# Kernel optimization log

Hardware: AMD Instinct MI355X
Metric: run time of the kernel (lower is better)

## Reference

```python
import jax, jax.numpy as jnp
import numpy as np

B, L, C, H = 8, 2048, 256, 4
D = C // H  # head_dim = 64
EPS = 1e-5


def setup_inputs() -> dict:
    key = jax.random.key(0)
    ks = jax.random.split(key, 16)
    s = lambda fan_in: 1.0 / np.sqrt(fan_in)
    inp = {
        'x0': jax.random.normal(ks[0], (B, L, C), jnp.float32),
        'x1': jax.random.normal(ks[1], (B, L, C), jnp.float32),
        # attention projections (stored as (in, out); torch Linear is x @ W.T + b)
        'Wqk': jax.random.normal(ks[2], (C, C), jnp.float32) * s(C),
        'bqk': jax.random.normal(ks[3], (C,), jnp.float32) * s(C),
        'Wv': jax.random.normal(ks[4], (C, C), jnp.float32) * s(C),
        'bv': jax.random.normal(ks[5], (C,), jnp.float32) * s(C),
        'Wout': jax.random.normal(ks[6], (C, C), jnp.float32) * s(C),
        'bout': jax.random.normal(ks[7], (C,), jnp.float32) * s(C),
        # shared FFN: Linear(2C->2C) -> LayerNorm -> GELU -> Linear(2C->C)
        'W1': jax.random.normal(ks[8], (2 * C, 2 * C), jnp.float32) * s(2 * C),
        'b1': jax.random.normal(ks[9], (2 * C,), jnp.float32) * s(2 * C),
        'ln_g': jnp.ones((2 * C,), jnp.float32),
        'ln_b': jnp.zeros((2 * C,), jnp.float32),
        'W2': jax.random.normal(ks[10], (2 * C, C), jnp.float32) * s(2 * C),
        'b2': jax.random.normal(ks[11], (C,), jnp.float32) * s(2 * C),
    }
    return inp


def _heads(t):
    # (B, L, C) -> (B, H, L, D)
    b, l, _ = t.shape
    return t.reshape(b, l, H, D).transpose(0, 2, 1, 3)


def _merge(t):
    # (B, H, L, D) -> (B, L, C)
    b, h, l, d = t.shape
    return t.transpose(0, 2, 1, 3).reshape(b, l, h * d)


def _ffn(z, W1, b1, ln_g, ln_b, W2, b2):
    h = z @ W1 + b1
    mu = jnp.mean(h, axis=-1, keepdims=True)
    var = jnp.var(h, axis=-1, keepdims=True)
    h = (h - mu) * jax.lax.rsqrt(var + EPS) * ln_g + ln_b
    h = jax.nn.gelu(h, approximate=False)
    return h @ W2 + b2


def reference(x0, x1, Wqk, bqk, Wv, bv, Wout, bout, W1, b1, ln_g, ln_b, W2, b2):
    scale_sqrt = D ** (-0.25)  # sqrt(head_dim**-0.5), applied to both sides
    qk0 = _heads(x0 @ Wqk + bqk) * scale_sqrt  # (B,H,M,D)
    qk1 = _heads(x1 @ Wqk + bqk) * scale_sqrt  # (B,H,N,D)
    v0 = _heads(x0 @ Wv + bv)
    v1 = _heads(x1 @ Wv + bv)

    # single shared similarity matrix (LightGlue trick)
    sim = jnp.einsum('bhid,bhjd->bhij', qk0, qk1)  # (B,H,M,N)
    attn01 = jax.nn.softmax(sim, axis=-1)           # rows: A->B
    attn10 = jax.nn.softmax(sim, axis=-2)           # cols: B->A (softmax of sim^T along last dim)
    m0 = jnp.einsum('bhij,bhjd->bhid', attn01, v1)  # (B,H,M,D)
    m1 = jnp.einsum('bhij,bhid->bhjd', attn10, v0)  # (B,H,N,D)

    m0 = _merge(m0) @ Wout + bout
    m1 = _merge(m1) @ Wout + bout

    x0_out = x0 + _ffn(jnp.concatenate([x0, m0], axis=-1), W1, b1, ln_g, ln_b, W2, b2)
    x1_out = x1 + _ffn(jnp.concatenate([x1, m1], axis=-1), W1, b1, ln_g, ln_b, W2, b2)
    return (x0_out, x1_out)
```

## Files before the change

### kernel.cpp

```cpp
#include <hip/hip_runtime.h>
#include <hip/hip_bf16.h>

typedef _Float16 f16;
typedef _Float16 f16x8 __attribute__((ext_vector_type(8)));
typedef _Float16 f16x4 __attribute__((ext_vector_type(4)));
typedef float f32x4 __attribute__((ext_vector_type(4)));

#define MFMA16(a, b, c) __builtin_amdgcn_mfma_f32_16x16x32_f16((a), (b), (c), 0, 0, 0)
#define MFMA16K16(a, b, c) __builtin_amdgcn_mfma_f32_16x16x16f16((a), (b), (c), 0, 0, 0)

__device__ __forceinline__ void load16(const void* g, void* l) {
    __builtin_amdgcn_global_load_lds((const __attribute__((address_space(1))) void*)g,
                                     (__attribute__((address_space(3))) void*)l, 16, 0, 0);
}

__global__ __launch_bounds__(256) void k_prep(const float* __restrict__ x0,
                                              const float* __restrict__ x1,
                                              const float* __restrict__ Wqk,
                                              const float* __restrict__ Wv,
                                              const float* __restrict__ W1,
                                              const float* __restrict__ W2,
                                              const float* __restrict__ Wout,
                                              const float* __restrict__ b1,
                                              const float* __restrict__ bout,
                                              f16* __restrict__ xh, f16* __restrict__ wcat_t,
                                              f16* __restrict__ w1t, f16* __restrict__ w1bt,
                                              f16* __restrict__ w2t, f16* __restrict__ woutf16,
                                              float* __restrict__ bias_eff) {
    __shared__ float red[4];
    const int blk = blockIdx.x, tid = threadIdx.x;
    if (blk < 8192) {
        size_t i = ((size_t)blk * 256 + tid) * 4;
        const float* src = (i < 4194304) ? (x0 + i) : (x1 + (i - 4194304));
        float4 v = *(const float4*)src;
        f16x4 o = {(f16)v.x, (f16)v.y, (f16)v.z, (f16)v.w};
        *(f16x4*)(xh + i) = o;
    } else if (blk < 8704) {
        int n = blk - 8192;
        const float* W = (n < 256) ? Wqk : Wv;
        wcat_t[n * 256 + tid] = (f16)W[tid * 256 + (n & 255)];
    } else if (blk < 9216) {
        int n = blk - 8704;
        w1t[n * 512 + tid] = (f16)W1[tid * 512 + n];
    } else if (blk < 9728) {
        int n = blk - 9216;
        w1bt[n * 256 + tid] = (f16)W1[(256 + tid) * 512 + n];
    } else if (blk < 10240) {
        int j = blk - 9728;
        int n = j >> 1, k = (j & 1) * 256 + tid;
        w2t[n * 512 + k] = (f16)W2[k * 256 + n];
    } else if (blk < 10496) {
        int o = (blk - 10240) * 256 + tid;
        woutf16[o] = (f16)Wout[o];
    } else {
        int n = blk - 10496;
        float s = bout[tid] * W1[(size_t)(256 + tid) * 512 + n];
#pragma unroll
        for (int off = 1; off < 64; off <<= 1) s += __shfl_xor(s, off);
        int wave = tid >> 6, lane = tid & 63;
        if (lane == 0) red[wave] = s;
        __syncthreads();
        if (tid == 0) bias_eff[n] = b1[n] + red[0] + red[1] + red[2] + red[3];
    }
}

__global__ __launch_bounds__(256) void k_gemm(const f16* __restrict__ A1,
                                              const f16* __restrict__ A2, int ksplit,
                                              int strideA, const f16* __restrict__ Bt, int K,
                                              int N, const float* __restrict__ bias1,
                                              const float* __restrict__ bias2, int mode,
                                              void* __restrict__ out1, void* __restrict__ out2,
                                              const float* __restrict__ res1,
                                              const float* __restrict__ res2) {
    const int bn0 = blockIdx.x * 128;
    const int bm0 = blockIdx.y * 128;
    __shared__ f16 As[2][4096];
    __shared__ f16 Bs[2][4096];
    const int tid = threadIdx.x;
    const int lane = tid & 63, wave = tid >> 6;
    const int quad = lane >> 4, l16 = lane & 15;
    const int wm0 = (wave & 1) * 64, wn0 = (wave >> 1) * 64;
    const int axor = l16 & 3;

    f32x4 acc[4][4];
#pragma unroll
    for (int tm = 0; tm < 4; tm++)
#pragma unroll
        for (int tn = 0; tn < 4; tn++) acc[tm][tn] = (f32x4){0.f, 0.f, 0.f, 0.f};

    auto stage = [&](int buf, int kt) {
        const int k0 = kt * 32;
        const f16* Ab = (k0 < ksplit) ? A1 : A2;
        const int koff = (k0 < ksplit) ? k0 : k0 - ksplit;
#pragma unroll
        for (int rd = 0; rd < 2; rd++) {
            const int cbase = rd * 256 + wave * 64;
            const int c = cbase + lane;
            const int row = c >> 2, col = (c & 3) ^ (row & 3);
            load16(Ab + (size_t)(bm0 + row) * strideA + koff + col * 8, &As[buf][cbase * 8]);
        }
#pragma unroll
        for (int rd = 0; rd < 2; rd++) {
            const int cbase = rd * 256 + wave * 64;
            const int c = cbase + lane;
            const int row = c >> 2, col = (c & 3) ^ (row & 3);
            load16(Bt + (size_t)(bn0 + row) * K + k0 + col * 8, &Bs[buf][cbase * 8]);
        }
    };

    const int NT = K >> 5;
    stage(0, 0);
    __syncthreads();
    for (int kt = 0; kt < NT; kt++) {
        const int cur = kt & 1;
        if (kt + 1 < NT) stage(cur ^ 1, kt + 1);
        f16x8 af[4], bf[4];
#pragma unroll
        for (int t = 0; t < 4; t++)
            af[t] = *(const f16x8*)&As[cur][(wm0 + t * 16 + l16) * 32 + (quad ^ axor) * 8];
#pragma unroll
        for (int t = 0; t < 4; t++)
            bf[t] = *(const f16x8*)&Bs[cur][(wn0 + t * 16 + l16) * 32 + (quad ^ axor) * 8];
#pragma unroll
        for (int tm = 0; tm < 4; tm++)
#pragma unroll
            for (int tn = 0; tn < 4; tn++) acc[tm][tn] = MFMA16(bf[tn], af[tm], acc[tm][tn]);
        __syncthreads();
    }

#pragma unroll
    for (int tm = 0; tm < 4; tm++) {
        const int m = bm0 + wm0 + tm * 16 + l16;
#pragma unroll
        for (int tn = 0; tn < 4; tn++) {
            const int n = bn0 + wn0 + tn * 16 + quad * 4;
            f32x4 v = acc[tm][tn];
            if (mode == 0) {
                const int s = m >> 14, r14 = m & 16383, b = r14 >> 11, l = r14 & 2047;
                if (n < 256) {
                    float4 bi = *(const float4*)(bias1 + n);
                    const int h = n >> 6, d = n & 63;
                    const size_t hh = (size_t)((s * 8 + b) * 4 + h);
                    f16x4 o = {(f16)((v[0] + bi.x) * 0.42466090f),
                               (f16)((v[1] + bi.y) * 0.42466090f),
                               (f16)((v[2] + bi.z) * 0.42466090f),
                               (f16)((v[3] + bi.w) * 0.42466090f)};
                    *(f16x4*)((f16*)out1 + (hh * 2048 + l) * 64 + d) = o;
                } else {
                    const int n2 = n - 256;
                    float4 bi = *(const float4*)(bias2 + n2);
                    const int h = n2 >> 6, d = n2 & 63;
                    const size_t hh = (size_t)((s * 8 + b) * 4 + h);
                    f16* o2 = (f16*)out2 + (hh * 64 + d) * 2048 + l;
                    o2[0] = (f16)(v[0] + bi.x);
                    o2[2048] = (f16)(v[1] + bi.y);
                    o2[4096] = (f16)(v[2] + bi.z);
                    o2[6144] = (f16)(v[3] + bi.w);
                }
            } else if (mode == 2) {
                float4 bi = *(const float4*)(bias1 + n);
                f16x4 o = {(f16)(v[0] + bi.x), (f16)(v[1] + bi.y), (f16)(v[2] + bi.z),
                           (f16)(v[3] + bi.w)};
                *(f16x4*)((f16*)out1 + (size_t)m * N + n) = o;
            } else if (mode == 3) {
                float4 bi = *(const float4*)(bias1 + n);
                const float* xr = (m < 16384) ? (res1 + (size_t)m * 256)
                                              : (res2 + (size_t)(m - 16384) * 256);
                float4 rr = *(const float4*)(xr + n);
                float4 o = {v[0] + bi.x + rr.x, v[1] + bi.y + rr.y, v[2] + bi.z + rr.z,
                            v[3] + bi.w + rr.w};
                *(float4*)((float*)out1 + (size_t)m * 256 + n) = o;
            } else {
                f16x4 o = {(f16)v[0], (f16)v[1], (f16)v[2], (f16)v[3]};
                *(f16x4*)((f16*)out1 + (size_t)m * 512 + 256 + n) = o;
            }
        }
    }
}

__global__ __launch_bounds__(256, 4) void k_flash(const f16* __restrict__ qkbuf,
                                                  const f16* __restrict__ vtbuf,
                                                  f16* __restrict__ mbuf) {
    const int z = blockIdx.z;
    const int bh = blockIdx.y;
    const int qt = blockIdx.x;
    const size_t HSZ = 2048 * 64;
    const size_t SSZ = 32 * HSZ;
    const f16* Q = qkbuf + (z ? SSZ : 0) + bh * HSZ;
    const f16* Kp = qkbuf + (z ? 0 : SSZ) + bh * HSZ;
    const f16* Vt = vtbuf + (z ? 0 : SSZ) + bh * HSZ;
    f16* Mo = mbuf + (size_t)z * (16384 * 256);

    __shared__ f16 Ks[2][4096];
    __shared__ f16 Vs[2][4096];

    const int tid = threadIdx.x, lane = tid & 63, wave = tid >> 6;
    const int quad = lane >> 4, l16 = lane & 15;
    const int srow = lane >> 3;
    const int slc = (lane & 7) ^ (srow & 7);

    const int q0 = qt * 128 + wave * 32;
    f16x8 qf[2][2];
#pragma unroll
    for (int tq = 0; tq < 2; tq++)
#pragma unroll
        for (int kk = 0; kk < 2; kk++)
            qf[tq][kk] =
                *(const f16x8*)(Q + (size_t)(q0 + tq * 16 + l16) * 64 + kk * 32 + quad * 8);

    auto stage = [&](int buf, int kv0) {
#pragma unroll
        for (int i = 0; i < 2; i++) {
            const int widx = wave * 2 + i;
            const int row = widx * 8 + srow;
            load16(Kp + (size_t)(kv0 + row) * 64 + slc * 8, &Ks[buf][widx * 512]);
            load16(Vt + (size_t)row * 2048 + kv0 + slc * 8, &Vs[buf][widx * 512]);
        }
    };

    f32x4 oacc[4][2];
#pragma unroll
    for (int td = 0; td < 4; td++)
#pragma unroll
        for (int tq = 0; tq < 2; tq++) oacc[td][tq] = (f32x4){0.f, 0.f, 0.f, 0.f};
    float lrow[2] = {0.f, 0.f};

    stage(0, 0);
    __syncthreads();

    for (int t = 0; t < 32; t++) {
        const int cur = t & 1;
        if (t < 31) stage(cur ^ 1, (t + 1) * 64);
        const f16* Kc = Ks[cur];
        const f16* Vc = Vs[cur];

        f32x4 sacc[4][2];
#pragma unroll
        for (int tkv = 0; tkv < 4; tkv++)
#pragma unroll
            for (int tq = 0; tq < 2; tq++) sacc[tkv][tq] = (f32x4){0.f, 0.f, 0.f, 0.f};
#pragma unroll
        for (int kk = 0; kk < 2; kk++) {
#pragma unroll
            for (int tkv = 0; tkv < 4; tkv++) {
                const int r = tkv * 16 + l16;
                f16x8 ka = *(const f16x8*)(Kc + r * 64 + (((kk * 4 + quad) ^ (r & 7)) * 8));
#pragma unroll
                for (int tq = 0; tq < 2; tq++)
                    sacc[tkv][tq] = MFMA16(ka, qf[tq][kk], sacc[tkv][tq]);
            }
        }

        f16x4 pk[4][2];
#pragma unroll
        for (int tq = 0; tq < 2; tq++) {
            float rs = 0.f;
#pragma unroll
            for (int tkv = 0; tkv < 4; tkv++) {
                float p0 = __builtin_amdgcn_exp2f(sacc[tkv][tq][0] - 8.0f);
                float p1 = __builtin_amdgcn_exp2f(sacc[tkv][tq][1] - 8.0f);
                float p2 = __builtin_amdgcn_exp2f(sacc[tkv][tq][2] - 8.0f);
                float p3 = __builtin_amdgcn_exp2f(sacc[tkv][tq][3] - 8.0f);
                pk[tkv][tq] = (f16x4){(f16)p0, (f16)p1, (f16)p2, (f16)p3};
                rs += (p0 + p1) + (p2 + p3);
            }
            lrow[tq] += rs;
        }

#pragma unroll
        for (int tkv = 0; tkv < 4; tkv++) {
#pragma unroll
            for (int td = 0; td < 4; td++) {
                const int r = td * 16 + l16;
                f16x4 va = *(const f16x4*)(Vc + r * 64 +
                                           (((2 * tkv + (quad >> 1)) ^ (r & 7)) * 8) +
                                           (quad & 1) * 4);
#pragma unroll
                for (int tq = 0; tq < 2; tq++)
                    oacc[td][tq] = MFMA16K16(va, pk[tkv][tq], oacc[td][tq]);
            }
        }
        __syncthreads();
    }

    const int b = bh >> 2, h = bh & 3;
#pragma unroll
    for (int tq = 0; tq < 2; tq++) {
        float ls = lrow[tq];
        ls += __shfl_xor(ls, 16);
        ls += __shfl_xor(ls, 32);
        const float inv = 1.f / ls;
        const int q = q0 + tq * 16 + l16;
        const size_t base = ((size_t)(b * 2048 + q)) * 256 + h * 64;
#pragma unroll
        for (int td = 0; td < 4; td++) {
            f16x4 o = {(f16)(oacc[td][tq][0] * inv), (f16)(oacc[td][tq][1] * inv),
                       (f16)(oacc[td][tq][2] * inv), (f16)(oacc[td][tq][3] * inv)};
            *(f16x4*)(Mo + base + td * 16 + quad * 4) = o;
        }
    }
}

__global__ __launch_bounds__(256) void k_ln_gelu(f16* __restrict__ h,
                                                 const float* __restrict__ g,
                                                 const float* __restrict__ bb) {
    const int tid = threadIdx.x, wave = tid >> 6, lane = tid & 63;
    const size_t row = (size_t)blockIdx.x * 4 + wave;
    f16* hr = h + row * 512 + lane * 8;
    f16x8 v = *(const f16x8*)hr;
    float x[8];
    float s = 0.f, sq = 0.f;
#pragma unroll
    for (int i = 0; i < 8; i++) {
        x[i] = (float)v[i];
        s += x[i];
        sq += x[i] * x[i];
    }
#pragma unroll
    for (int off = 1; off < 64; off <<= 1) {
        s += __shfl_xor(s, off);
        sq += __shfl_xor(sq, off);
    }
    const float mu = s * (1.f / 512.f);
    const float var = sq * (1.f / 512.f) - mu * mu;
    const float rstd = rsqrtf(var + 1e-5f);
    float4 g0 = *(const float4*)(g + lane * 8), g1 = *(const float4*)(g + lane * 8 + 4);
    float4 b0 = *(const float4*)(bb + lane * 8), b1 = *(const float4*)(bb + lane * 8 + 4);
    float gg[8] = {g0.x, g0.y, g0.z, g0.w, g1.x, g1.y, g1.z, g1.w};
    float bv[8] = {b0.x, b0.y, b0.z, b0.w, b1.x, b1.y, b1.z, b1.w};
#pragma unroll
    for (int i = 0; i < 8; i++) {
        float a = (x[i] - mu) * rstd * gg[i] + bv[i];
        a = 0.5f * a * (1.f + erff(a * 0.70710678118f));
        v[i] = (f16)a;
    }
    *(f16x8*)hr = v;
}


extern "C" void kernel_launch(void* const* d_in, const int* in_sizes, int n_in, void* d_out,
                              int out_size, void* d_ws, size_t ws_size, hipStream_t stream) {
    const float* x0 = (const float*)d_in[0];
    const float* x1 = (const float*)d_in[1];
    const float* Wqk = (const float*)d_in[2];
    const float* bqk = (const float*)d_in[3];
    const float* Wv = (const float*)d_in[4];
    const float* bv = (const float*)d_in[5];
    const float* Wout = (const float*)d_in[6];
    const float* bout = (const float*)d_in[7];
    const float* W1 = (const float*)d_in[8];
    const float* b1 = (const float*)d_in[9];
    const float* lng = (const float*)d_in[10];
    const float* lnb = (const float*)d_in[11];
    const float* W2 = (const float*)d_in[12];
    const float* b2 = (const float*)d_in[13];
    float* out = (float*)d_out;

    char* ws = (char*)d_ws;
    f16* xh = (f16*)(ws);
    f16* qk = (f16*)(ws + 16777216);
    f16* vt = (f16*)(ws + 33554432);
    f16* mbuf = (f16*)(ws + 50331648);
    f16* hbuf = qk;
    f16* w1bt = (f16*)(ws + 16777216);
    f16* woutf16 = w1bt + 131072;
    f16* wcat_t = (f16*)(ws + 67108864);
    f16* w1t = wcat_t + 131072;
    f16* w2t = w1t + 262144;
    float* bias_eff = (float*)(w2t + 131072);

    k_prep<<<11008, 256, 0, stream>>>(x0, x1, Wqk, Wv, W1, W2, Wout, b1, bout, xh, wcat_t, w1t,
                                      w1bt, w2t, woutf16, bias_eff);
    k_gemm<<<dim3(2, 4), 256, 0, stream>>>(w1bt, w1bt, 1 << 30, 256, woutf16, 256, 256, nullptr,
                                           nullptr, 4, w1t, nullptr, nullptr, nullptr);
    k_gemm<<<dim3(4, 256), 256, 0, stream>>>(xh, xh, 1 << 30, 256, wcat_t, 256, 512, bqk, bv, 0,
                                             qk, vt, nullptr, nullptr);
    k_flash<<<dim3(16, 32, 2), 256, 0, stream>>>(qk, vt, mbuf);
    k_gemm<<<dim3(4, 256), 256, 0, stream>>>(xh, mbuf, 256, 256, w1t, 512, 512, bias_eff,
                                             nullptr, 2, hbuf, nullptr, nullptr, nullptr);
    k_ln_gelu<<<8192, 256, 0, stream>>>(hbuf, lng, lnb);
    k_gemm<<<dim3(2, 256), 256, 0, stream>>>(hbuf, hbuf, 1 << 30, 512, w2t, 512, 256, b2, nullptr,
                                             3, out, nullptr, x0, x1);
}
```

Before: 327.3 us.

## Fold Wout into W1 inside prep, swap grid axes, use fp16 residual

Removes the separate small GEMM that folded Wout into W1 and computes that product directly in the prep kernel with per-thread dot products over shared memory. Swaps grid dimensions so consecutive blocks iterate over row tiles and heads, altering scheduling and L2 reuse. The final GEMM epilogue reads the fp16 copy of the inputs for the residual instead of fp32, reducing traffic at the cost of residual precision.

```diff
diff --git a/kernel.cpp b/kernel.cpp
--- a/kernel.cpp
+++ b/kernel.cpp
@@ -24,9 +24,9 @@
                                               const float* __restrict__ b1,
                                               const float* __restrict__ bout,
                                               f16* __restrict__ xh, f16* __restrict__ wcat_t,
-                                              f16* __restrict__ w1t, f16* __restrict__ w1bt,
-                                              f16* __restrict__ w2t, f16* __restrict__ woutf16,
+                                              f16* __restrict__ w1t, f16* __restrict__ w2t,
                                               float* __restrict__ bias_eff) {
+    __shared__ float lbuf[256];
     __shared__ float red[4];
     const int blk = blockIdx.x, tid = threadIdx.x;
     if (blk < 8192) {
@@ -43,17 +43,20 @@
         int n = blk - 8704;
         w1t[n * 512 + tid] = (f16)W1[tid * 512 + n];
     } else if (blk < 9728) {
-        int n = blk - 9216;
-        w1bt[n * 256 + tid] = (f16)W1[(256 + tid) * 512 + n];
-    } else if (blk < 10240) {
-        int j = blk - 9728;
+        int j = blk - 9216;
         int n = j >> 1, k = (j & 1) * 256 + tid;
         w2t[n * 512 + k] = (f16)W2[k * 256 + n];
-    } else if (blk < 10496) {
-        int o = (blk - 10240) * 256 + tid;
-        woutf16[o] = (f16)Wout[o];
+    } else if (blk < 10240) {
+        int n = blk - 9728;
+        lbuf[tid] = W1[(size_t)(256 + tid) * 512 + n];
+        __syncthreads();
+        const float* wr = Wout + (size_t)tid * 256;
+        float s = 0.f;
+#pragma unroll 8
+        for (int t = 0; t < 256; t++) s += lbuf[t] * wr[t];
+        w1t[n * 512 + 256 + tid] = (f16)s;
     } else {
-        int n = blk - 10496;
+        int n = blk - 10240;
         float s = bout[tid] * W1[(size_t)(256 + tid) * 512 + n];
 #pragma unroll
         for (int off = 1; off < 64; off <<= 1) s += __shfl_xor(s, off);
@@ -70,10 +73,9 @@
                                               int N, const float* __restrict__ bias1,
                                               const float* __restrict__ bias2, int mode,
                                               void* __restrict__ out1, void* __restrict__ out2,
-                                              const float* __restrict__ res1,
-                                              const float* __restrict__ res2) {
-    const int bn0 = blockIdx.x * 128;
-    const int bm0 = blockIdx.y * 128;
+                                              const f16* __restrict__ resh) {
+    const int bm0 = blockIdx.x * 128;
+    const int bn0 = blockIdx.y * 128;
     __shared__ f16 As[2][4096];
     __shared__ f16 Bs[2][4096];
     const int tid = threadIdx.x;
@@ -162,17 +164,12 @@
                 f16x4 o = {(f16)(v[0] + bi.x), (f16)(v[1] + bi.y), (f16)(v[2] + bi.z),
                            (f16)(v[3] + bi.w)};
                 *(f16x4*)((f16*)out1 + (size_t)m * N + n) = o;
-            } else if (mode == 3) {
+            } else {
                 float4 bi = *(const float4*)(bias1 + n);
-                const float* xr = (m < 16384) ? (res1 + (size_t)m * 256)
-                                              : (res2 + (size_t)(m - 16384) * 256);
-                float4 rr = *(const float4*)(xr + n);
-                float4 o = {v[0] + bi.x + rr.x, v[1] + bi.y + rr.y, v[2] + bi.z + rr.z,
-                            v[3] + bi.w + rr.w};
+                f16x4 rr = *(const f16x4*)(resh + (size_t)m * 256 + n);
+                float4 o = {v[0] + bi.x + (float)rr[0], v[1] + bi.y + (float)rr[1],
+                            v[2] + bi.z + (float)rr[2], v[3] + bi.w + (float)rr[3]};
                 *(float4*)((float*)out1 + (size_t)m * 256 + n) = o;
-            } else {
-                f16x4 o = {(f16)v[0], (f16)v[1], (f16)v[2], (f16)v[3]};
-                *(f16x4*)((f16*)out1 + (size_t)m * 512 + 256 + n) = o;
             }
         }
     }
@@ -182,8 +179,8 @@
                                                   const f16* __restrict__ vtbuf,
                                                   f16* __restrict__ mbuf) {
     const int z = blockIdx.z;
-    const int bh = blockIdx.y;
-    const int qt = blockIdx.x;
+    const int bh = blockIdx.x;
+    const int qt = blockIdx.y;
     const size_t HSZ = 2048 * 64;
     const size_t SSZ = 32 * HSZ;
     const f16* Q = qkbuf + (z ? SSZ : 0) + bh * HSZ;
@@ -362,23 +359,19 @@
     f16* vt = (f16*)(ws + 33554432);
     f16* mbuf = (f16*)(ws + 50331648);
     f16* hbuf = qk;
-    f16* w1bt = (f16*)(ws + 16777216);
-    f16* woutf16 = w1bt + 131072;
     f16* wcat_t = (f16*)(ws + 67108864);
     f16* w1t = wcat_t + 131072;
     f16* w2t = w1t + 262144;
     float* bias_eff = (float*)(w2t + 131072);
 
-    k_prep<<<11008, 256, 0, stream>>>(x0, x1, Wqk, Wv, W1, W2, Wout, b1, bout, xh, wcat_t, w1t,
-                                      w1bt, w2t, woutf16, bias_eff);
-    k_gemm<<<dim3(2, 4), 256, 0, stream>>>(w1bt, w1bt, 1 << 30, 256, woutf16, 256, 256, nullptr,
-                                           nullptr, 4, w1t, nullptr, nullptr, nullptr);
-    k_gemm<<<dim3(4, 256), 256, 0, stream>>>(xh, xh, 1 << 30, 256, wcat_t, 256, 512, bqk, bv, 0,
-                                             qk, vt, nullptr, nullptr);
-    k_flash<<<dim3(16, 32, 2), 256, 0, stream>>>(qk, vt, mbuf);
-    k_gemm<<<dim3(4, 256), 256, 0, stream>>>(xh, mbuf, 256, 256, w1t, 512, 512, bias_eff,
-                                             nullptr, 2, hbuf, nullptr, nullptr, nullptr);
+    k_prep<<<10752, 256, 0, stream>>>(x0, x1, Wqk, Wv, W1, W2, Wout, b1, bout, xh, wcat_t, w1t,
+                                      w2t, bias_eff);
+    k_gemm<<<dim3(256, 4), 256, 0, stream>>>(xh, xh, 1 << 30, 256, wcat_t, 256, 512, bqk, bv, 0,
+                                             qk, vt, nullptr);
+    k_flash<<<dim3(32, 16, 2), 256, 0, stream>>>(qk, vt, mbuf);
+    k_gemm<<<dim3(256, 4), 256, 0, stream>>>(xh, mbuf, 256, 256, w1t, 512, 512, bias_eff,
+                                             nullptr, 2, hbuf, nullptr, nullptr);
     k_ln_gelu<<<8192, 256, 0, stream>>>(hbuf, lng, lnb);
-    k_gemm<<<dim3(2, 256), 256, 0, stream>>>(hbuf, hbuf, 1 << 30, 512, w2t, 512, 256, b2, nullptr,
-                                             3, out, nullptr, x0, x1);
-}
+    k_gemm<<<dim3(256, 2), 256, 0, stream>>>(hbuf, hbuf, 1 << 30, 512, w2t, 512, 256, b2,
+                                             nullptr, 3, out, nullptr, xh);
+}
```

New measurement: 357.1 us. 9.1% more time.
